# Performance work log

Hardware: AMD Instinct MI355X
Metric: run time of the kernel (lower is better)

## Reference

```python
import jax, jax.numpy as jnp
import numpy as np

TAU = 0.1
NEG = -1000000.0
B, S, E, H, O = 64, 512, 256, 512, 256  # batch, seq, embed_size, n_hidden, out_size


def _lstm_direction(x, W_ih, W_hh, b_ih, b_hh, reverse):
    # x: [S, B, 2E]; W_ih: [4H, 2E]; W_hh: [4H, H]
    xg = jnp.einsum('sbe,ge->sbg', x, W_ih) + b_ih + b_hh  # precompute input gates [S,B,4H]
    if reverse:
        xg = xg[::-1]
    n_b = x.shape[1]
    n_h = W_hh.shape[1]
    h0 = jnp.zeros((n_b, n_h), x.dtype)
    c0 = jnp.zeros((n_b, n_h), x.dtype)

    def step(carry, g_x):
        h, c = carry
        g = g_x + h @ W_hh.T
        i, f, gg, o = jnp.split(g, 4, axis=-1)  # torch gate order: i, f, g, o
        i = jax.nn.sigmoid(i)
        f = jax.nn.sigmoid(f)
        gg = jnp.tanh(gg)
        o = jax.nn.sigmoid(o)
        c = f * c + i * gg
        h = o * jnp.tanh(c)
        return (h, c), h

    _, hs = jax.lax.scan(step, (h0, c0), xg)
    return hs[::-1] if reverse else hs  # [S, B, H]


def setup_inputs() -> dict:
    key = jax.random.key(0)
    ks = jax.random.split(key, 12)
    s = 0.05
    return {
        'inputs': jax.random.normal(ks[0], (B, S, 2, E), jnp.float32),
        'W_ih_f': jax.random.normal(ks[1], (4 * H, 2 * E), jnp.float32) * s,
        'W_hh_f': jax.random.normal(ks[2], (4 * H, H), jnp.float32) * s,
        'b_ih_f': jax.random.normal(ks[3], (4 * H,), jnp.float32) * s,
        'b_hh_f': jax.random.normal(ks[4], (4 * H,), jnp.float32) * s,
        'W_ih_b': jax.random.normal(ks[5], (4 * H, 2 * E), jnp.float32) * s,
        'W_hh_b': jax.random.normal(ks[6], (4 * H, H), jnp.float32) * s,
        'b_ih_b': jax.random.normal(ks[7], (4 * H,), jnp.float32) * s,
        'b_hh_b': jax.random.normal(ks[8], (4 * H,), jnp.float32) * s,
        'W_out': jax.random.normal(ks[9], (O, 2 * H), jnp.float32) * s,
        'b_out': jax.random.normal(ks[10], (O,), jnp.float32) * s,
    }


def reference(inputs, W_ih_f, W_hh_f, b_ih_f, b_hh_f,
              W_ih_b, W_hh_b, b_ih_b, b_hh_b, W_out, b_out):
    b, s = inputs.shape[0], inputs.shape[1]
    x = inputs.reshape(b, s, -1).transpose(1, 0, 2)  # [S, B, 2E]
    hf = _lstm_direction(x, W_ih_f, W_hh_f, b_ih_f, b_hh_f, reverse=False)
    hb = _lstm_direction(x, W_ih_b, W_hh_b, b_ih_b, b_hh_b, reverse=True)
    out = jnp.concatenate([hf, hb], axis=-1).transpose(1, 0, 2)  # [B, S, 2H]
    d = out.shape[-1]
    scores = jnp.einsum('bsd,btd->bst', out, out) / jnp.sqrt(jnp.asarray(d, out.dtype))
    scores = jnp.where(scores > TAU, scores, jnp.asarray(NEG, out.dtype))  # data-dependent threshold mask
    weights = jax.nn.softmax(scores, axis=-1)
    context = jnp.einsum('bst,btd->bsd', weights, out)  # [B, S, 2H]
    y = context[:, -1, :] @ W_out.T + b_out  # only last position feeds the output layer
    return y.reshape(b, 1, 1, -1)
```

## Files before the change

### kernel.cpp

```cpp
#include <hip/hip_runtime.h>
#include <hip/hip_cooperative_groups.h>
#include <hip/hip_bf16.h>

#define RFL(x) __builtin_amdgcn_readfirstlane(x)

typedef __attribute__((ext_vector_type(8))) short bf16x8;
typedef __attribute__((ext_vector_type(4))) float f32x4;

__device__ __forceinline__ float sigm(float x) { return 1.0f / (1.0f + __expf(-x)); }

__device__ __forceinline__ ushort bf16_rne(float x) {
  __hip_bfloat16 h = __float2bfloat16(x);
  return *reinterpret_cast<ushort*>(&h);
}
__device__ __forceinline__ float bf16_tof(ushort u) {
  __hip_bfloat16 h = *reinterpret_cast<__hip_bfloat16*>(&u);
  return __bfloat162float(h);
}

__device__ __forceinline__ unsigned long long ld_agent_u64(const void* p) {
  return __hip_atomic_load((unsigned long long*)p, __ATOMIC_RELAXED, __HIP_MEMORY_SCOPE_AGENT);
}
__device__ __forceinline__ unsigned int ld_agent_u32(const unsigned int* p) {
  return __hip_atomic_load(p, __ATOMIC_RELAXED, __HIP_MEMORY_SCOPE_AGENT);
}
__device__ __forceinline__ float ld_agent_f32(const float* p) {
  return __hip_atomic_load((float*)p, __ATOMIC_RELAXED, __HIP_MEMORY_SCOPE_AGENT);
}
__device__ __forceinline__ void st_agent_u32(unsigned int* p, unsigned int v) {
  __hip_atomic_store(p, v, __ATOMIC_RELAXED, __HIP_MEMORY_SCOPE_AGENT);
}
__device__ __forceinline__ void st_agent_f32(float* p, float v) {
  __hip_atomic_store(p, v, __ATOMIC_RELAXED, __HIP_MEMORY_SCOPE_AGENT);
}
__device__ __forceinline__ void st_agent_u16(ushort* p, ushort v) {
  __hip_atomic_store(p, v, __ATOMIC_RELAXED, __HIP_MEMORY_SCOPE_AGENT);
}

__device__ __forceinline__ unsigned long long ld_l2_u64(const void* p) {
  return *(volatile const unsigned long long*)p;
}
__device__ __forceinline__ unsigned int ld_l2_u32(const unsigned int* p) {
  return *(volatile const unsigned int*)p;
}
__device__ __forceinline__ void st_l2_u32(unsigned int* p, unsigned int v) {
  *(volatile unsigned int*)p = v;
}

__device__ __forceinline__ unsigned int xcc_id() {
  unsigned int x;
  asm volatile("s_getreg_b32 %0, hwreg(HW_REG_XCC_ID)" : "=s"(x));
  return x;
}

__global__ void __launch_bounds__(256) kw_split2(const float* __restrict__ Whh_f,
    const float* __restrict__ Whh_b, const float* __restrict__ Wih_f,
    const float* __restrict__ Wih_b, ushort* __restrict__ WBS) {
  int idx = blockIdx.x * 256 + threadIdx.x;
  int m = idx >> 18;
  int r = (idx >> 7) & 2047;
  int k4 = idx & 127;
  const float* W = (m == 0) ? Whh_f : (m == 1) ? Whh_b : (m == 2) ? Wih_f : Wih_b;
  float4 v = *(const float4*)&W[(size_t)r * 512 + k4 * 4];
  ushort h0 = bf16_rne(v.x), h1 = bf16_rne(v.y), h2 = bf16_rne(v.z), h3 = bf16_rne(v.w);
  ushort l0 = bf16_rne(v.x - bf16_tof(h0));
  ushort l1 = bf16_rne(v.y - bf16_tof(h1));
  ushort l2 = bf16_rne(v.z - bf16_tof(h2));
  ushort l3 = bf16_rne(v.w - bf16_tof(h3));
  ushort* base = WBS + (size_t)m * 2048 * 1024 + (size_t)r * 1024;
  uint2 HI = { (uint)h0 | ((uint)h1 << 16), (uint)h2 | ((uint)h3 << 16) };
  uint2 LO = { (uint)l0 | ((uint)l1 << 16), (uint)l2 | ((uint)l3 << 16) };
  *(uint2*)(base + k4 * 4) = HI;
  *(uint2*)(base + 512 + k4 * 4) = LO;
}

template<bool AGENT>
__device__ __forceinline__ void xg_produce(const ushort* __restrict__ WBS,
    const float* __restrict__ inputs,
    const float* __restrict__ bih_f, const float* __restrict__ bhh_f,
    const float* __restrict__ bih_b, const float* __restrict__ bhh_b,
    float* __restrict__ XGo, float* part,
    int d, int jt, int cx, int tlb, int tle, int tid, int kq, int l15, int l4) {
  bf16x8 Afr[4][4];
  const ushort* WB = WBS + (size_t)(2 + d) * 2048 * 1024;
  const int c32s[4] = { 2*kq, 2*kq + 1, 16 + 2*kq, 16 + 2*kq + 1 };
#pragma unroll
  for (int g = 0; g < 4; ++g)
#pragma unroll
    for (int s = 0; s < 4; ++s)
      Afr[g][s] = *(const bf16x8*)(WB + (size_t)(g * 512 + jt * 16 + l15) * 1024 + c32s[s] * 32 + 8 * l4);

  int jj_g = tid & 15, b_g = tid >> 4;
  int j_g = jt * 16 + jj_g;
  const float* bih = d ? bih_b : bih_f;
  const float* bhh = d ? bhh_b : bhh_f;
  float bias[4];
#pragma unroll
  for (int g = 0; g < 4; ++g) bias[g] = bih[g * 512 + j_g] + bhh[g * 512 + j_g];

#pragma unroll 1
  for (int tl = tlb; tl < tle; ++tl) {
    int t = cx + tl;
    int pos = d ? (511 - t) : t;
    bf16x8 Bfr[4][4];
#pragma unroll
    for (int bt = 0; bt < 4; ++bt) {
      const float* bp = inputs + ((size_t)(bt * 16 + l15) * 512 + pos) * 512;
#pragma unroll
      for (int q = 0; q < 2; ++q) {
        int k0 = (2 * kq + q) * 32 + 8 * l4;
        float4 x0 = *(const float4*)(bp + k0);
        float4 x1 = *(const float4*)(bp + k0 + 4);
        float xv[8] = { x0.x, x0.y, x0.z, x0.w, x1.x, x1.y, x1.z, x1.w };
        union { bf16x8 v; ushort u[8]; } H, L;
#pragma unroll
        for (int e = 0; e < 8; ++e) {
          ushort hh = bf16_rne(xv[e]);
          H.u[e] = hh;
          L.u[e] = bf16_rne(xv[e] - bf16_tof(hh));
        }
        Bfr[bt][q] = H.v;
        Bfr[bt][2 + q] = L.v;
      }
    }
    f32x4 acc[4][4];
#pragma unroll
    for (int g = 0; g < 4; ++g)
#pragma unroll
      for (int bt = 0; bt < 4; ++bt) acc[g][bt] = (f32x4){0.f, 0.f, 0.f, 0.f};
#pragma unroll
    for (int pass = 0; pass < 2; ++pass) {
#pragma unroll
      for (int s = 0; s < 4; ++s) {
        int bs2 = pass ? (s ^ 2) : s;
#pragma unroll
        for (int g = 0; g < 4; ++g)
#pragma unroll
          for (int bt = 0; bt < 4; ++bt)
            acc[g][bt] = __builtin_amdgcn_mfma_f32_16x16x32_bf16(
                Afr[g][s], Bfr[bt][bs2], acc[g][bt], 0, 0, 0);
      }
    }
    __syncthreads();
#pragma unroll
    for (int g = 0; g < 4; ++g)
#pragma unroll
      for (int bt = 0; bt < 4; ++bt) {
        int w = ((kq * 4 + g) * 64 + bt * 16 + l15) * 20 + 4 * l4;
        *(f32x4*)&part[w] = acc[g][bt];
      }
    __syncthreads();
    size_t xgb = (size_t)(d * 32 + tl) * 64;
#pragma unroll
    for (int u = 0; u < 2; ++u) {
      int b = b_g + 32 * u;
#pragma unroll
      for (int g = 0; g < 4; ++g) {
        float pre = bias[g];
#pragma unroll
        for (int kqi = 0; kqi < 8; ++kqi)
          pre += part[((kqi * 4 + g) * 64 + b) * 20 + jj_g];
        if (AGENT) st_agent_f32(&XGo[(xgb + b) * 2048 + g * 512 + j_g], pre);
        else       XGo[(xgb + b) * 2048 + g * 512 + j_g] = pre;
      }
    }
  }
}

__global__ void __launch_bounds__(512, 1) k1_pro(const ushort* __restrict__ WBS,
    const float* __restrict__ inputs,
    const float* __restrict__ bih_f, const float* __restrict__ bhh_f,
    const float* __restrict__ bih_b, const float* __restrict__ bhh_b,
    float* __restrict__ XGo) {
  extern __shared__ float part[];
  int bid = blockIdx.x;
  int tid = threadIdx.x;
  int kq = RFL((int)(tid >> 6));
  int lane = tid & 63, l15 = lane & 15, l4 = lane >> 4;
  int jt = bid & 31, d = (bid >> 5) & 1, ts = bid >> 6;
  xg_produce<false>(WBS, inputs, bih_f, bhh_f, bih_b, bhh_b, XGo, part,
                    d, jt, 0, ts * 8, ts * 8 + 8, tid, kq, l15, l4);
}

__global__ void __launch_bounds__(512, 1) k2_fused(const ushort* __restrict__ WBS,
    const float* __restrict__ inputs, float* __restrict__ XGa, float* __restrict__ XGb,
    ushort* __restrict__ HTB, float* __restrict__ OUTT, float* __restrict__ Cws,
    unsigned int* __restrict__ Bar,
    const float* __restrict__ bih_f, const float* __restrict__ bhh_f,
    const float* __restrict__ bih_b, const float* __restrict__ bhh_b) {
  extern __shared__ float part[];
  int bid = blockIdx.x;
  int tid = threadIdx.x;
  int kq = RFL((int)(tid >> 6));
  int lane = tid & 63;
  int l15 = lane & 15, l4 = lane >> 4;
  int r = bid & 7;

  unsigned int* prodS = Bar + 4096;
  unsigned int* consS = Bar + 8192;

  if (r >= 4) {
    int pid = (bid >> 3) * 4 + (r - 4);
    int d = pid & 1, jt = (pid >> 1) & 31, th = pid >> 6;
#pragma unroll 1
    for (int c = 1; c < 16; ++c) {
      if (tid < 64) {
        unsigned int v; int gg = 0;
        do {
          unsigned int a = ld_agent_u32(&consS[(lane * 2) * 16]);
          unsigned int b2 = ld_agent_u32(&consS[(lane * 2 + 1) * 16]);
          v = a < b2 ? a : b2;
          if (v < (unsigned int)(c - 1)) __builtin_amdgcn_s_sleep(8);
        } while (!__all((int)(v >= (unsigned int)(c - 1))) && ++gg < (1 << 16));
      }
      __syncthreads();
      float* xw = (c & 1) ? XGb : XGa;
      xg_produce<true>(WBS, inputs, bih_f, bhh_f, bih_b, bhh_b, xw, part,
                       d, jt, c * 32, th * 16, th * 16 + 16, tid, kq, l15, l4);
      __syncthreads();
      if (tid == 0) st_agent_u32(&prodS[pid * 16], (unsigned int)c);
    }
    return;
  }

  int d = r & 1, bs = r >> 1;
  int jt = bid >> 3;
  int cid = (bid >> 3) * 4 + r;
  const int c32s[4] = { 2*kq, 2*kq + 1, 16 + 2*kq, 16 + 2*kq + 1 };

  bf16x8 Afr[4][4];
  const ushort* WB = WBS + (size_t)d * 2048 * 1024;
#pragma unroll
  for (int g = 0; g < 4; ++g)
#pragma unroll
    for (int s = 0; s < 4; ++s)
      Afr[g][s] = *(const bf16x8*)(WB + (size_t)(g * 512 + jt * 16 + l15) * 1024 + c32s[s] * 32 + 8 * l4);

  int jj_g = tid & 15, b_l = tid >> 4;
  int j_g = jt * 16 + jj_g;
  int bcol = bs * 32 + b_l;
  float cc = 0.f;

  int jl4 = jj_g >> 2, jreg = jj_g & 3;
  int btr = b_l >> 4;
  int rsw = (b_l & 15) ^ (jl4 << 2);
  int rbase = jl4 * 16 + rsw;

  unsigned int* slots = Bar + (size_t)r * 512;
  unsigned int* XTab  = Bar + 2048;
  int* flagsh = (int*)(part + 20480);

  unsigned int myx = xcc_id() + 1u;
  if (tid == 0) { st_agent_u32(&XTab[bid], myx); flagsh[0] = 1; }
  __syncthreads();
  if (tid < 64) {
    int k = lane & 31;
    unsigned int q; int gg = 0;
    do { q = ld_agent_u32(&XTab[r + 8 * k]); } while (q == 0u && ++gg < (1 << 20));
    if (!__all((int)(q == myx)) && lane == 0) flagsh[0] = 0;
  }
  __syncthreads();
  int fastu = RFL(flagsh[0]);
  __syncthreads();

  int pslot = lane & 31;
  bool own = (pslot == jt);

#pragma unroll 1
  for (int c = 0; c < 16; ++c) {
    if (c > 0) {
      if (tid < 64) {
        unsigned int v; int gg = 0;
        do {
          unsigned int a = ld_agent_u32(&prodS[(lane * 2) * 16]);
          unsigned int b2 = ld_agent_u32(&prodS[(lane * 2 + 1) * 16]);
          v = a < b2 ? a : b2;
        } while (!__all((int)(v >= (unsigned int)c)) && ++gg < (1 << 16));
      }
      __syncthreads();
    }
    const float* xgp = (c & 1) ? XGb : XGa;

#pragma unroll 1
    for (int tl = 0; tl < 32; ++tl) {
      int t = c * 32 + tl, p = t & 1;
      float xg[4];
      {
        size_t xb = ((size_t)(d * 32 + tl) * 64 + bcol) * 2048;
#pragma unroll
        for (int g = 0; g < 4; ++g)
          xg[g] = ld_agent_f32(&xgp[xb + g * 512 + j_g]);
      }
      {
        unsigned int v; int gg = 0;
        if (fastu) {
          do { v = own ? 0xFFFFFFFFu : ld_l2_u32(&slots[pslot * 16]); }
          while (!__all((int)(v >= (unsigned int)t)) && ++gg < (1 << 13));
        } else {
          do { v = own ? 0xFFFFFFFFu : ld_agent_u32(&slots[pslot * 16]); }
          while (!__all((int)(v >= (unsigned int)t)) && ++gg < (1 << 13));
        }
      }
      const ushort* hb = HTB + (size_t)(p * 2 + d) * 65536;
      bf16x8 Bfr[2][4];
#pragma unroll
      for (int bt = 0; bt < 2; ++bt)
#pragma unroll
        for (int s = 0; s < 4; ++s) {
          const ushort* fp = hb + (size_t)c32s[s] * 2048 + (bs * 32 + bt * 16 + l15) * 32 + 8 * l4;
          union { bf16x8 v; unsigned long long q[2]; } u;
          if (fastu) { u.q[0] = ld_l2_u64(fp); u.q[1] = ld_l2_u64(fp + 4); }
          else       { u.q[0] = ld_agent_u64(fp); u.q[1] = ld_agent_u64(fp + 4); }
          Bfr[bt][s] = u.v;
        }
      f32x4 acc[4][2];
#pragma unroll
      for (int g = 0; g < 4; ++g)
#pragma unroll
        for (int bt = 0; bt < 2; ++bt) acc[g][bt] = (f32x4){0.f, 0.f, 0.f, 0.f};
#pragma unroll
      for (int pass = 0; pass < 2; ++pass) {
#pragma unroll
        for (int s = 0; s < 4; ++s) {
          int bs2 = pass ? (s ^ 2) : s;
#pragma unroll
          for (int g = 0; g < 4; ++g)
#pragma unroll
            for (int bt = 0; bt < 2; ++bt)
              acc[g][bt] = __builtin_amdgcn_mfma_f32_16x16x32_bf16(
                  Afr[g][s], Bfr[bt][bs2], acc[g][bt], 0, 0, 0);
        }
      }
#pragma unroll
      for (int g = 0; g < 4; ++g)
#pragma unroll
        for (int bt = 0; bt < 2; ++bt) {
          int f4i = ((kq * 4 + g) * 2 + bt) * 64 + l4 * 16 + (l15 ^ (l4 << 2));
          *(f32x4*)&part[f4i * 4] = acc[g][bt];
        }
      __syncthreads();
      float pre[4];
#pragma unroll
      for (int g = 0; g < 4; ++g) {
        float a = xg[g];
#pragma unroll
        for (int kqi = 0; kqi < 8; ++kqi)
          a += part[(((kqi * 4 + g) * 2 + btr) * 64 + rbase) * 4 + jreg];
        pre[g] = a;
      }
      float ig = sigm(pre[0]), fg = sigm(pre[1]), gv = tanhf(pre[2]), og = sigm(pre[3]);
      cc = fmaf(fg, cc, ig * gv);
      float hval = og * tanhf(cc);
      ushort hh = bf16_rne(hval);
      ushort hl = bf16_rne(hval - bf16_tof(hh));
      ushort* hbn = HTB + (size_t)((p ^ 1) * 2 + d) * 65536;
      size_t hoff = (size_t)(j_g >> 5) * 2048 + (size_t)bcol * 32 + (j_g & 31);
      if (fastu) { hbn[hoff] = hh; hbn[hoff + 16 * 2048] = hl; }
      else { st_agent_u16(hbn + hoff, hh); st_agent_u16(hbn + hoff + 16 * 2048, hl); }
      __syncthreads();
      if (tid == 0) {
        if (fastu) st_l2_u32(&slots[jt * 16], (unsigned int)(t + 1));
        else       st_agent_u32(&slots[jt * 16], (unsigned int)(t + 1));
      }
      int pos = d ? (511 - t) : t;
      OUTT[((size_t)(d * 512 + pos) * 512 + j_g) * 64 + bcol] = hval;
    }
    if (tid == 0) st_agent_u32(&consS[cid * 16], (unsigned int)(c + 1));
  }
  Cws[(size_t)(d * 512 + j_g) * 64 + bcol] = cc;
}

__global__ void __launch_bounds__(256) k3a_scores(const float* __restrict__ OUTT, float* __restrict__ ST) {
  int wid = RFL((int)(threadIdx.x >> 6));
  int b = threadIdx.x & 63;
  int t = blockIdx.x * 4 + wid;
  float acc = 0.f;
  for (int dd = 0; dd < 2; ++dd) {
    size_t bt = (size_t)(dd * 512 + t)   * 512;
    size_t bl = (size_t)(dd * 512 + 511) * 512;
    for (int jj = 0; jj < 512; ++jj)
      acc = fmaf(OUTT[(bt + jj) * 64 + b], OUTT[(bl + jj) * 64 + b], acc);
  }
  float sc = acc * (1.0f / 32.0f);
  ST[t * 64 + b] = (sc > 0.1f) ? sc : -1000000.0f;
}

__global__ void __launch_bounds__(64) k3b_softmax(const float* __restrict__ ST, float* __restrict__ WT) {
  int b = threadIdx.x;
  float mx = -3.0e38f;
  for (int t = 0; t < 512; ++t) mx = fmaxf(mx, ST[t * 64 + b]);
  float sum = 0.f;
  for (int t = 0; t < 512; ++t) sum += __expf(ST[t * 64 + b] - mx);
  float inv = 1.0f / sum;
  for (int t = 0; t < 512; ++t) WT[t * 64 + b] = __expf(ST[t * 64 + b] - mx) * inv;
}

__global__ void __launch_bounds__(256) k3c_ctx(const float* __restrict__ OUTT,
    const float* __restrict__ WT, float* __restrict__ CTX) {
  int bq = blockIdx.x;
  int d = bq >> 7, j0 = (bq & 127) * 4;
  int wid = RFL((int)(threadIdx.x >> 6));
  int b = threadIdx.x & 63;
  int j = j0 + wid;
  float acc = 0.f;
  for (int t = 0; t < 512; ++t)
    acc = fmaf(WT[t * 64 + b], OUTT[((size_t)(d * 512 + t) * 512 + j) * 64 + b], acc);
  CTX[(size_t)(d * 512 + j) * 64 + b] = acc;
}

__global__ void __launch_bounds__(256) k3dpre(const float* __restrict__ Wout, float* __restrict__ WoT) {
  int o = threadIdx.x;
  int k0 = blockIdx.x * 64;
  for (int k = k0; k < k0 + 64; ++k)
    WoT[k * 256 + o] = Wout[(size_t)o * 1024 + k];
}

__global__ void __launch_bounds__(256) k3d_y(const float* __restrict__ CTX,
    const float* __restrict__ WoT, const float* __restrict__ bout, float* __restrict__ y) {
  __shared__ float lc[1024];
  int b = blockIdx.x, o = threadIdx.x;
  for (int k = threadIdx.x; k < 1024; k += 256) lc[k] = CTX[(size_t)k * 64 + b];
  __syncthreads();
  float acc = bout[o];
  for (int k = 0; k < 1024; ++k) acc = fmaf(lc[k], WoT[k * 256 + o], acc);
  y[b * 256 + o] = acc;
}

extern "C" void kernel_launch(void* const* d_in, const int* in_sizes, int n_in,
                              void* d_out, int out_size, void* d_ws, size_t ws_size,
                              hipStream_t stream) {
  (void)in_sizes; (void)n_in; (void)out_size; (void)ws_size;
  const float* inputs = (const float*)d_in[0];
  const float* Wih_f = (const float*)d_in[1];
  const float* Whh_f = (const float*)d_in[2];
  const float* bih_f = (const float*)d_in[3];
  const float* bhh_f = (const float*)d_in[4];
  const float* Wih_b = (const float*)d_in[5];
  const float* Whh_b = (const float*)d_in[6];
  const float* bih_b = (const float*)d_in[7];
  const float* bhh_b = (const float*)d_in[8];
  const float* Wout  = (const float*)d_in[9];
  const float* bout  = (const float*)d_in[10];
  float* y = (float*)d_out;

  float* ws = (float*)d_ws;
  size_t off = 0;
  float* XGa = ws + off; off += (size_t)2 * 32 * 2048 * 64;
  float* XGb = ws + off; off += (size_t)2 * 32 * 2048 * 64;
  float* OUTT= ws + off; off += (size_t)2 * 512 * 512 * 64;
  ushort* HTB = (ushort*)(ws + off); off += (size_t)2 * 2 * 64 * 512;
  float* Cws = ws + off; off += (size_t)2 * 512 * 64;
  float* ST  = ws + off; off += (size_t)512 * 64;
  float* WT  = ws + off; off += (size_t)512 * 64;
  float* CTX = ws + off; off += (size_t)2 * 512 * 64;
  float* WoT = ws + off; off += (size_t)1024 * 256;
  ushort* WBS = (ushort*)(ws + off); off += (size_t)4 * 2048 * 1024 / 2;
  unsigned int* Bar = (unsigned int*)(ws + off); off += 16384;

  hipMemsetAsync(HTB, 0, (size_t)4 * 65536 * sizeof(ushort), stream);
  hipMemsetAsync(Cws, 0, (size_t)2 * 512 * 64 * sizeof(float), stream);
  hipMemsetAsync(Bar, 0, 65536, stream);

  const int ldsK = 8 * 4 * 64 * 20 * 4;
  hipFuncSetAttribute(reinterpret_cast<const void*>(k2_fused),
                      hipFuncAttributeMaxDynamicSharedMemorySize, ldsK);
  hipFuncSetAttribute(reinterpret_cast<const void*>(k1_pro),
                      hipFuncAttributeMaxDynamicSharedMemorySize, ldsK);

  kw_split2<<<4096, 256, 0, stream>>>(Whh_f, Whh_b, Wih_f, Wih_b, WBS);
  k1_pro<<<256, 512, ldsK, stream>>>(WBS, inputs, bih_f, bhh_f, bih_b, bhh_b, XGa);

  void* args[] = { (void*)&WBS, (void*)&inputs, (void*)&XGa, (void*)&XGb,
                   (void*)&HTB, (void*)&OUTT, (void*)&Cws, (void*)&Bar,
                   (void*)&bih_f, (void*)&bhh_f, (void*)&bih_b, (void*)&bhh_b };
  hipLaunchCooperativeKernel(reinterpret_cast<void*>(k2_fused),
                             dim3(256), dim3(512), args, ldsK, stream);

  k3a_scores<<<128, 256, 0, stream>>>(OUTT, ST);
  k3b_softmax<<<1, 64, 0, stream>>>(ST, WT);
  k3c_ctx<<<256, 256, 0, stream>>>(OUTT, WT, CTX);
  k3dpre<<<16, 256, 0, stream>>>(Wout, WoT);
  k3d_y<<<64, 256, 0, stream>>>(CTX, WoT, bout, y);
}
```

Before: 3.148 ms.

## Merge both LSTM directions into each recurrent consumer block, add more producer blocks

Each recurrent consumer block now runs both the forward and backward direction. It keeps two sets of W_hh fragments in registers and steps the two directions in turn within each timestep. This halves the number of consumer blocks per group and frees slots for input-gate producer blocks, which rise from 4 to 6 per group of 8; each producer now covers about 11 timesteps instead of 16. The aim is to overlap one direction's sync wait with the other direction's compute and to raise input-projection throughput. The cost is roughly double the serial work per block per timestep and higher register pressure.

```diff
diff --git a/kernel.cpp b/kernel.cpp
--- a/kernel.cpp
+++ b/kernel.cpp
@@ -196,58 +196,60 @@
   int l15 = lane & 15, l4 = lane >> 4;
   int r = bid & 7;
 
+  unsigned int* XTab  = Bar + 2048;
   unsigned int* prodS = Bar + 4096;
   unsigned int* consS = Bar + 8192;
 
-  if (r >= 4) {
-    int pid = (bid >> 3) * 4 + (r - 4);
+  if (r >= 2) {
+    int pid = (bid >> 3) * 6 + (r - 2);
     int d = pid & 1, jt = (pid >> 1) & 31, th = pid >> 6;
+    int tlb = th * 11;
+    int tle = tlb + 11; if (tle > 32) tle = 32;
 #pragma unroll 1
     for (int c = 1; c < 16; ++c) {
       if (tid < 64) {
         unsigned int v; int gg = 0;
         do {
-          unsigned int a = ld_agent_u32(&consS[(lane * 2) * 16]);
-          unsigned int b2 = ld_agent_u32(&consS[(lane * 2 + 1) * 16]);
-          v = a < b2 ? a : b2;
+          v = ld_agent_u32(&consS[lane * 16]);
           if (v < (unsigned int)(c - 1)) __builtin_amdgcn_s_sleep(8);
         } while (!__all((int)(v >= (unsigned int)(c - 1))) && ++gg < (1 << 16));
       }
       __syncthreads();
       float* xw = (c & 1) ? XGb : XGa;
       xg_produce<true>(WBS, inputs, bih_f, bhh_f, bih_b, bhh_b, xw, part,
-                       d, jt, c * 32, th * 16, th * 16 + 16, tid, kq, l15, l4);
+                       d, jt, c * 32, tlb, tle, tid, kq, l15, l4);
       __syncthreads();
       if (tid == 0) st_agent_u32(&prodS[pid * 16], (unsigned int)c);
     }
     return;
   }
 
-  int d = r & 1, bs = r >> 1;
+  int bs = r;
   int jt = bid >> 3;
-  int cid = (bid >> 3) * 4 + r;
+  int cid = jt * 2 + bs;
   const int c32s[4] = { 2*kq, 2*kq + 1, 16 + 2*kq, 16 + 2*kq + 1 };
 
-  bf16x8 Afr[4][4];
-  const ushort* WB = WBS + (size_t)d * 2048 * 1024;
-#pragma unroll
-  for (int g = 0; g < 4; ++g)
-#pragma unroll
-    for (int s = 0; s < 4; ++s)
-      Afr[g][s] = *(const bf16x8*)(WB + (size_t)(g * 512 + jt * 16 + l15) * 1024 + c32s[s] * 32 + 8 * l4);
+  bf16x8 Afr[2][4][4];
+#pragma unroll
+  for (int dd = 0; dd < 2; ++dd) {
+    const ushort* WB = WBS + (size_t)dd * 2048 * 1024;
+#pragma unroll
+    for (int g = 0; g < 4; ++g)
+#pragma unroll
+      for (int s = 0; s < 4; ++s)
+        Afr[dd][g][s] = *(const bf16x8*)(WB + (size_t)(g * 512 + jt * 16 + l15) * 1024 + c32s[s] * 32 + 8 * l4);
+  }
 
   int jj_g = tid & 15, b_l = tid >> 4;
   int j_g = jt * 16 + jj_g;
   int bcol = bs * 32 + b_l;
-  float cc = 0.f;
+  float cc[2] = { 0.f, 0.f };
 
   int jl4 = jj_g >> 2, jreg = jj_g & 3;
   int btr = b_l >> 4;
   int rsw = (b_l & 15) ^ (jl4 << 2);
   int rbase = jl4 * 16 + rsw;
 
-  unsigned int* slots = Bar + (size_t)r * 512;
-  unsigned int* XTab  = Bar + 2048;
   int* flagsh = (int*)(part + 20480);
 
   unsigned int myx = xcc_id() + 1u;
@@ -272,9 +274,10 @@
       if (tid < 64) {
         unsigned int v; int gg = 0;
         do {
-          unsigned int a = ld_agent_u32(&prodS[(lane * 2) * 16]);
-          unsigned int b2 = ld_agent_u32(&prodS[(lane * 2 + 1) * 16]);
-          v = a < b2 ? a : b2;
+          unsigned int a0 = ld_agent_u32(&prodS[(lane * 3) * 16]);
+          unsigned int a1 = ld_agent_u32(&prodS[(lane * 3 + 1) * 16]);
+          unsigned int a2 = ld_agent_u32(&prodS[(lane * 3 + 2) * 16]);
+          v = a0 < a1 ? a0 : a1; v = v < a2 ? v : a2;
         } while (!__all((int)(v >= (unsigned int)c)) && ++gg < (1 << 16));
       }
       __syncthreads();
@@ -284,90 +287,98 @@
 #pragma unroll 1
     for (int tl = 0; tl < 32; ++tl) {
       int t = c * 32 + tl, p = t & 1;
-      float xg[4];
-      {
-        size_t xb = ((size_t)(d * 32 + tl) * 64 + bcol) * 2048;
+      float xg[2][4];
+#pragma unroll
+      for (int dd = 0; dd < 2; ++dd) {
+        size_t xb = ((size_t)(dd * 32 + tl) * 64 + bcol) * 2048;
 #pragma unroll
         for (int g = 0; g < 4; ++g)
-          xg[g] = ld_agent_f32(&xgp[xb + g * 512 + j_g]);
-      }
-      {
-        unsigned int v; int gg = 0;
-        if (fastu) {
-          do { v = own ? 0xFFFFFFFFu : ld_l2_u32(&slots[pslot * 16]); }
-          while (!__all((int)(v >= (unsigned int)t)) && ++gg < (1 << 13));
-        } else {
-          do { v = own ? 0xFFFFFFFFu : ld_agent_u32(&slots[pslot * 16]); }
-          while (!__all((int)(v >= (unsigned int)t)) && ++gg < (1 << 13));
+          xg[dd][g] = ld_agent_f32(&xgp[xb + g * 512 + j_g]);
+      }
+
+#pragma unroll
+      for (int dd = 0; dd < 2; ++dd) {
+        unsigned int* slots = Bar + (size_t)(dd * 2 + bs) * 512;
+        {
+          unsigned int v; int gg = 0;
+          if (fastu) {
+            do { v = own ? 0xFFFFFFFFu : ld_l2_u32(&slots[pslot * 16]); }
+            while (!__all((int)(v >= (unsigned int)t)) && ++gg < (1 << 14));
+          } else {
+            do { v = own ? 0xFFFFFFFFu : ld_agent_u32(&slots[pslot * 16]); }
+            while (!__all((int)(v >= (unsigned int)t)) && ++gg < (1 << 14));
+          }
         }
-      }
-      const ushort* hb = HTB + (size_t)(p * 2 + d) * 65536;
-      bf16x8 Bfr[2][4];
-#pragma unroll
-      for (int bt = 0; bt < 2; ++bt)
-#pragma unroll
-        for (int s = 0; s < 4; ++s) {
-          const ushort* fp = hb + (size_t)c32s[s] * 2048 + (bs * 32 + bt * 16 + l15) * 32 + 8 * l4;
-          union { bf16x8 v; unsigned long long q[2]; } u;
-          if (fastu) { u.q[0] = ld_l2_u64(fp); u.q[1] = ld_l2_u64(fp + 4); }
-          else       { u.q[0] = ld_agent_u64(fp); u.q[1] = ld_agent_u64(fp + 4); }
-          Bfr[bt][s] = u.v;
+        const ushort* hb = HTB + (size_t)(p * 2 + dd) * 65536;
+        bf16x8 Bfr[2][4];
+#pragma unroll
+        for (int bt = 0; bt < 2; ++bt)
+#pragma unroll
+          for (int s = 0; s < 4; ++s) {
+            const ushort* fp = hb + (size_t)c32s[s] * 2048 + (bs * 32 + bt * 16 + l15) * 32 + 8 * l4;
+            union { bf16x8 v; unsigned long long q[2]; } u;
+            if (fastu) { u.q[0] = ld_l2_u64(fp); u.q[1] = ld_l2_u64(fp + 4); }
+            else       { u.q[0] = ld_agent_u64(fp); u.q[1] = ld_agent_u64(fp + 4); }
+            Bfr[bt][s] = u.v;
+          }
+        f32x4 acc[4][2];
+#pragma unroll
+        for (int g = 0; g < 4; ++g)
+#pragma unroll
+          for (int bt = 0; bt < 2; ++bt) acc[g][bt] = (f32x4){0.f, 0.f, 0.f, 0.f};
+#pragma unroll
+        for (int pass = 0; pass < 2; ++pass) {
+#pragma unroll
+          for (int s = 0; s < 4; ++s) {
+            int bs2 = pass ? (s ^ 2) : s;
+#pragma unroll
+            for (int g = 0; g < 4; ++g)
+#pragma unroll
+              for (int bt = 0; bt < 2; ++bt)
+                acc[g][bt] = __builtin_amdgcn_mfma_f32_16x16x32_bf16(
+                    Afr[dd][g][s], Bfr[bt][bs2], acc[g][bt], 0, 0, 0);
+          }
         }
-      f32x4 acc[4][2];
-#pragma unroll
-      for (int g = 0; g < 4; ++g)
-#pragma unroll
-        for (int bt = 0; bt < 2; ++bt) acc[g][bt] = (f32x4){0.f, 0.f, 0.f, 0.f};
-#pragma unroll
-      for (int pass = 0; pass < 2; ++pass) {
-#pragma unroll
-        for (int s = 0; s < 4; ++s) {
-          int bs2 = pass ? (s ^ 2) : s;
-#pragma unroll
-          for (int g = 0; g < 4; ++g)
-#pragma unroll
-            for (int bt = 0; bt < 2; ++bt)
-              acc[g][bt] = __builtin_amdgcn_mfma_f32_16x16x32_bf16(
-                  Afr[g][s], Bfr[bt][bs2], acc[g][bt], 0, 0, 0);
+#pragma unroll
+        for (int g = 0; g < 4; ++g)
+#pragma unroll
+          for (int bt = 0; bt < 2; ++bt) {
+            int f4i = ((kq * 4 + g) * 2 + bt) * 64 + l4 * 16 + (l15 ^ (l4 << 2));
+            *(f32x4*)&part[f4i * 4] = acc[g][bt];
+          }
+        __syncthreads();
+        float pre[4];
+#pragma unroll
+        for (int g = 0; g < 4; ++g) {
+          float a = xg[dd][g];
+#pragma unroll
+          for (int kqi = 0; kqi < 8; ++kqi)
+            a += part[(((kqi * 4 + g) * 2 + btr) * 64 + rbase) * 4 + jreg];
+          pre[g] = a;
         }
-      }
-#pragma unroll
-      for (int g = 0; g < 4; ++g)
-#pragma unroll
-        for (int bt = 0; bt < 2; ++bt) {
-          int f4i = ((kq * 4 + g) * 2 + bt) * 64 + l4 * 16 + (l15 ^ (l4 << 2));
-          *(f32x4*)&part[f4i * 4] = acc[g][bt];
+        float ig = sigm(pre[0]), fg = sigm(pre[1]), gv = tanhf(pre[2]), og = sigm(pre[3]);
+        cc[dd] = fmaf(fg, cc[dd], ig * gv);
+        float hval = og * tanhf(cc[dd]);
+        ushort hh = bf16_rne(hval);
+        ushort hl = bf16_rne(hval - bf16_tof(hh));
+        ushort* hbn = HTB + (size_t)((p ^ 1) * 2 + dd) * 65536;
+        size_t hoff = (size_t)(j_g >> 5) * 2048 + (size_t)bcol * 32 + (j_g & 31);
+        if (fastu) { hbn[hoff] = hh; hbn[hoff + 16 * 2048] = hl; }
+        else { st_agent_u16(hbn + hoff, hh); st_agent_u16(hbn + hoff + 16 * 2048, hl); }
+        __syncthreads();
+        if (tid == 0) {
+          if (fastu) st_l2_u32(&slots[jt * 16], (unsigned int)(t + 1));
+          else       st_agent_u32(&slots[jt * 16], (unsigned int)(t + 1));
         }
-      __syncthreads();
-      float pre[4];
-#pragma unroll
-      for (int g = 0; g < 4; ++g) {
-        float a = xg[g];
-#pragma unroll
-        for (int kqi = 0; kqi < 8; ++kqi)
-          a += part[(((kqi * 4 + g) * 2 + btr) * 64 + rbase) * 4 + jreg];
-        pre[g] = a;
-      }
-      float ig = sigm(pre[0]), fg = sigm(pre[1]), gv = tanhf(pre[2]), og = sigm(pre[3]);
-      cc = fmaf(fg, cc, ig * gv);
-      float hval = og * tanhf(cc);
-      ushort hh = bf16_rne(hval);
-      ushort hl = bf16_rne(hval - bf16_tof(hh));
-      ushort* hbn = HTB + (size_t)((p ^ 1) * 2 + d) * 65536;
-      size_t hoff = (size_t)(j_g >> 5) * 2048 + (size_t)bcol * 32 + (j_g & 31);
-      if (fastu) { hbn[hoff] = hh; hbn[hoff + 16 * 2048] = hl; }
-      else { st_agent_u16(hbn + hoff, hh); st_agent_u16(hbn + hoff + 16 * 2048, hl); }
-      __syncthreads();
-      if (tid == 0) {
-        if (fastu) st_l2_u32(&slots[jt * 16], (unsigned int)(t + 1));
-        else       st_agent_u32(&slots[jt * 16], (unsigned int)(t + 1));
-      }
-      int pos = d ? (511 - t) : t;
-      OUTT[((size_t)(d * 512 + pos) * 512 + j_g) * 64 + bcol] = hval;
+        int pos = dd ? (511 - t) : t;
+        OUTT[((size_t)(dd * 512 + pos) * 512 + j_g) * 64 + bcol] = hval;
+      }
     }
     if (tid == 0) st_agent_u32(&consS[cid * 16], (unsigned int)(c + 1));
   }
-  Cws[(size_t)(d * 512 + j_g) * 64 + bcol] = cc;
+#pragma unroll
+  for (int dd = 0; dd < 2; ++dd)
+    Cws[(size_t)(dd * 512 + j_g) * 64 + bcol] = cc[dd];
 }
 
 __global__ void __launch_bounds__(256) k3a_scores(const float* __restrict__ OUTT, float* __restrict__ ST) {
```

New measurement: 5.574 ms. 77.1% more time.
